# Performance work log

Hardware: AMD Instinct MI355X
Metric: run time of the kernel (lower is better)

Reference implementation:

```python
import jax, jax.numpy as jnp
import numpy as np

FILTER_LEN = 32
SCALE = float(np.sqrt(10 ** (-15 / 10)))  # expected_SI_power_dB = -15


def _fir_valid(x, w):
    """Valid cross-correlation along W axis. x: [B,H,W,1], w: [L] -> [B,H,W-L+1,1].
    Matches Keras Conv2D(kernel_size=(1,L), padding='valid') (cross-correlation)."""
    B, H, W, _ = x.shape
    L = w.shape[0]
    xr = x.reshape(B * H, W, 1)
    k = w.reshape(L, 1, 1)  # (spatial, in, out)
    y = jax.lax.conv_general_dilated(xr, k, window_strides=(1,), padding='VALID',
                                     dimension_numbers=('NWC', 'WIO', 'NWC'))
    return y.reshape(B, H, W - L + 1, 1)


def setup_inputs() -> dict:
    key = jax.random.key(0)
    ks = jax.random.split(key, 10)
    B, H, W = 16, 1, 262144
    f32 = jnp.float32
    return {
        'x_real': jax.random.normal(ks[0], (B, H, W, 1), f32),
        'x_imag': jax.random.normal(ks[1], (B, H, W, 1), f32),
        'w1_pre': jax.random.normal(ks[2], (1, 8), f32) * 0.5,
        'w2_pre': jax.random.normal(ks[3], (8, 1), f32) * 0.5,
        'w_fir_r': jax.random.normal(ks[4], (FILTER_LEN,), f32) * 0.1,
        'w_fir_i': jax.random.normal(ks[5], (FILTER_LEN,), f32) * 0.1,
        'w1_post': jax.random.normal(ks[6], (1, 8), f32) * 0.5,
        'b1_post': jax.random.normal(ks[7], (8,), f32) * 0.1,
        'w2_post': jax.random.normal(ks[8], (8, 1), f32) * 0.5,
        'b2_post': jax.random.normal(ks[9], (1,), f32) * 0.1,
    }


def reference(x_real, x_imag, w1_pre, w2_pre, w_fir_r, w_fir_i,
              w1_post, b1_post, w2_post, b2_post):
    # --- pre nonlinearity on magnitude (1x1 conv MLP: 1 -> 8 tanh -> 1) ---
    x_mag = jnp.sqrt(x_real * x_real + x_imag * x_imag)      # [B,H,W,1]
    x_phase = jnp.arctan2(x_imag, x_real)                    # [B,H,W,1]
    h = jnp.tanh(jnp.einsum('bhwc,cf->bhwf', x_mag, w1_pre))  # [B,H,W,8]
    m = jnp.einsum('bhwf,fc->bhwc', h, w2_pre)               # [B,H,W,1]
    xh_r = m * jnp.cos(x_phase)
    xh_i = m * jnp.sin(x_phase)
    # --- complex FIR (length-32, valid) via 4 real convs ---
    zr = _fir_valid(xh_r, w_fir_r) - _fir_valid(xh_i, w_fir_i)
    zi = _fir_valid(xh_i, w_fir_r) + _fir_valid(xh_r, w_fir_i)
    # --- post nonlinearity on magnitude (1x1 conv MLP: 1 -> 8 relu -> 1) ---
    z_mag = jnp.sqrt(zr * zr + zi * zi)
    z_phase = jnp.arctan2(zi, zr)
    g = jax.nn.relu(jnp.einsum('bhwc,cf->bhwf', z_mag, w1_post) + b1_post)
    zm = jnp.einsum('bhwf,fc->bhwc', g, w2_post) + b2_post
    yr = SCALE * zm * jnp.cos(z_phase)
    yi = SCALE * zm * jnp.sin(z_phase)
    # complex output represented as [real, imag] on last axis: [B,H,W-31,2]
    return jnp.concatenate([yr, yi], axis=-1)
```

## Files before the change

### kernel.cpp

```cpp
#include <hip/hip_runtime.h>

#define TILE   2048
#define WTILE  512
#define NSW    560
#define WIDTH  262144
#define OUTW   (WIDTH - 31)
#define SCALE_V 0.17782794100389229f

#define TBL_N    1024
#define TBL_MAX  10.0f
#define TBL_SCL  (TBL_N / TBL_MAX)

typedef _Float16 half8  __attribute__((ext_vector_type(8)));
typedef _Float16 half4v __attribute__((ext_vector_type(4)));
typedef float    floatx4 __attribute__((ext_vector_type(4)));

__device__ __forceinline__ float wload(const float* __restrict__ w, int t) {
    return (t >= 0 && t < 32) ? w[t] : 0.0f;
}

#define MFMA16(A, B, C) __builtin_amdgcn_mfma_f32_16x16x32_f16((A), (B), (C), 0, 0, 0)

__device__ __forceinline__ float s_of_mag(float mag, const float* w1, const float* w2) {
    if (mag == 0.0f) {
        float s = 0.f;
#pragma unroll
        for (int f = 0; f < 8; ++f) s = fmaf(w2[f], w1[f], s);
        return s;
    }
    float m = 0.f;
#pragma unroll
    for (int f = 0; f < 8; ++f) m = fmaf(w2[f], tanhf(w1[f] * mag), m);
    return m / mag;
}

__global__ void fill_s_table(const float* __restrict__ w1_pre,
                             const float* __restrict__ w2_pre,
                             float2* __restrict__ tbl)
{
    const int i = blockIdx.x * 256 + threadIdx.x;
    if (i >= TBL_N) return;
    float w1[8], w2[8];
#pragma unroll
    for (int f = 0; f < 8; ++f) { w1[f] = w1_pre[f]; w2[f] = w2_pre[f]; }
    const float m0 = (float)i       * (1.0f / TBL_SCL);
    const float m1 = (float)(i + 1) * (1.0f / TBL_SCL);
    const float s0 = s_of_mag(m0, w1, w2);
    const float s1 = s_of_mag(m1, w1, w2);
    tbl[i] = make_float2(s0, s1 - s0);
}

__global__ __launch_bounds__(256) void fused_hammer_mfma(
    const float* __restrict__ xr_g,   const float* __restrict__ xi_g,
    const float* __restrict__ w1_pre, const float* __restrict__ w2_pre,
    const float* __restrict__ wfr,    const float* __restrict__ wfi,
    const float* __restrict__ w1_post,const float* __restrict__ b1_post,
    const float* __restrict__ w2_post,const float* __restrict__ b2_post,
    const float2* __restrict__ tbl_g,
    float* __restrict__ out)
{
    __shared__ __align__(16) _Float16 s_rh[4][NSW];
    __shared__ __align__(16) _Float16 s_rl[4][NSW];
    __shared__ __align__(16) _Float16 s_ih[4][NSW];
    __shared__ __align__(16) _Float16 s_il[4][NSW];
    __shared__ __align__(16) float2   s_tab[TBL_N];

    const int tid    = threadIdx.x;
    const int lane   = tid & 63;
    const int wv     = tid >> 6;
    const int tstart = blockIdx.x * TILE;
    const int wstart = tstart + wv * WTILE;
    const int brow   = blockIdx.y;
    const long rowbase = (long)brow * WIDTH;

    {
        const float4* src = (const float4*)tbl_g;
#pragma unroll
        for (int q = 0; q < 2; ++q) {
            const int idx = 2 * tid + q;
            ((float4*)s_tab)[idx] = src[idx];
        }
    }

    float w1p[8], b1p[8], w2p[8];
#pragma unroll
    for (int f = 0; f < 8; ++f) { w1p[f] = w1_post[f]; b1p[f] = b1_post[f]; w2p[f] = w2_post[f]; }
    const float b2p = b2_post[0];

    const int jA = lane & 15;
    const int kg = lane >> 4;
    half8 A1r_h, A1r_l, A1mi_h, A1mi_l, A1i_h, A1i_l, A2r_h, A2r_l, A2i_h, A2i_l;
#pragma unroll
    for (int jj = 0; jj < 8; ++jj) {
        const int k  = 8 * kg + jj;
        const int t1 = k - jA;
        const float wr1 = wload(wfr, t1);
        const float wi1 = wload(wfi, t1);
        const int t2 = (k < 16) ? (k + 32 - jA) : (k + 16 - jA);
        const float wr2 = wload(wfr, t2);
        const float wi2 = wload(wfi, t2);
        const float a2r = (k < 16) ? wr2 : -wi2;
        const float a2i = (k < 16) ? wi2 : wr2;
        _Float16 h;
        h = (_Float16)wr1;   A1r_h[jj]  = h; A1r_l[jj]  = (_Float16)(wr1 - (float)h);
        h = (_Float16)(-wi1);A1mi_h[jj] = h; A1mi_l[jj] = (_Float16)(-wi1 - (float)h);
        h = (_Float16)wi1;   A1i_h[jj]  = h; A1i_l[jj]  = (_Float16)(wi1 - (float)h);
        h = (_Float16)a2r;   A2r_h[jj]  = h; A2r_l[jj]  = (_Float16)(a2r - (float)h);
        h = (_Float16)a2i;   A2i_h[jj]  = h; A2i_l[jj]  = (_Float16)(a2i - (float)h);
    }

    __syncthreads();

    for (int p = lane; p < NSW / 4; p += 64) {
        const int g = wstart + 4 * p;
        float4 vr, vi;
        if (g + 3 < WIDTH) {
            vr = *(const float4*)(xr_g + rowbase + g);
            vi = *(const float4*)(xi_g + rowbase + g);
        } else {
            float rr[4], ii[4];
#pragma unroll
            for (int e = 0; e < 4; ++e) {
                const int gg = g + e;
                rr[e] = (gg < WIDTH) ? xr_g[rowbase + gg] : 0.f;
                ii[e] = (gg < WIDTH) ? xi_g[rowbase + gg] : 0.f;
            }
            vr = make_float4(rr[0], rr[1], rr[2], rr[3]);
            vi = make_float4(ii[0], ii[1], ii[2], ii[3]);
        }
        const float* vrf = &vr.x;
        const float* vif = &vi.x;
        half4v rh, rl, ih, il;
#pragma unroll
        for (int e = 0; e < 4; ++e) {
            const float r  = vrf[e], im = vif[e];
            const float sq  = fmaf(r, r, im * im);
            const float mag = __builtin_sqrtf(sq);
            const float t   = fminf(mag * TBL_SCL, (float)(TBL_N - 2) + 0.999f);
            const int   i0  = (int)t;
            const float frac = t - (float)i0;
            const float2 en = s_tab[i0];
            const float s   = fmaf(frac, en.y, en.x);
            const float xhr = s * r;
            const float xhi = s * im;
            const _Float16 hr = (_Float16)xhr;
            const _Float16 hi = (_Float16)xhi;
            rh[e] = hr; rl[e] = (_Float16)(xhr - (float)hr);
            ih[e] = hi; il[e] = (_Float16)(xhi - (float)hi);
        }
        *(half4v*)&s_rh[wv][4 * p] = rh;
        *(half4v*)&s_rl[wv][4 * p] = rl;
        *(half4v*)&s_ih[wv][4 * p] = ih;
        *(half4v*)&s_il[wv][4 * p] = il;
    }
    asm volatile("s_waitcnt lgkmcnt(0)" ::: "memory");

    const bool row_aligned = ((brow & 1) == 0);

#pragma unroll
    for (int tt = 0; tt < 2; ++tt) {
        const int base_o = 256 * tt;
        const int i1 = base_o + 16 * jA + 8 * kg;
        const half8 Bxr_h = *(const half8*)&s_rh[wv][i1];
        const half8 Bxi_h = *(const half8*)&s_ih[wv][i1];
        const half8 Bxr_l = *(const half8*)&s_rl[wv][i1];
        const half8 Bxi_l = *(const half8*)&s_il[wv][i1];
        const int i2 = base_o + 16 * jA + 32 + 8 * (kg & 1);
        const _Float16* srcH = (kg < 2) ? s_rh[wv] : s_ih[wv];
        const _Float16* srcL = (kg < 2) ? s_rl[wv] : s_il[wv];
        const half8 Bmx_h = *(const half8*)&srcH[i2];
        const half8 Bmx_l = *(const half8*)&srcL[i2];

        floatx4 accr = {0.f, 0.f, 0.f, 0.f};
        floatx4 acci = {0.f, 0.f, 0.f, 0.f};
        accr = MFMA16(A1r_h,  Bxr_h, accr);  acci = MFMA16(A1i_h,  Bxr_h, acci);
        accr = MFMA16(A1mi_h, Bxi_h, accr);  acci = MFMA16(A1r_h,  Bxi_h, acci);
        accr = MFMA16(A2r_h,  Bmx_h, accr);  acci = MFMA16(A2i_h,  Bmx_h, acci);
        accr = MFMA16(A1r_h,  Bxr_l, accr);  acci = MFMA16(A1i_h,  Bxr_l, acci);
        accr = MFMA16(A1mi_h, Bxi_l, accr);  acci = MFMA16(A1r_h,  Bxi_l, acci);
        accr = MFMA16(A2r_h,  Bmx_l, accr);  acci = MFMA16(A2i_h,  Bmx_l, acci);
        accr = MFMA16(A1r_l,  Bxr_h, accr);  acci = MFMA16(A1i_l,  Bxr_h, acci);
        accr = MFMA16(A1mi_l, Bxi_h, accr);  acci = MFMA16(A1r_l,  Bxi_h, acci);
        accr = MFMA16(A2r_l,  Bmx_h, accr);  acci = MFMA16(A2i_l,  Bmx_h, acci);

        const int obase = wstart + base_o + 16 * jA + 4 * kg;
        float ox[8];
#pragma unroll
        for (int r = 0; r < 4; ++r) {
            const float zr  = accr[r], zi = acci[r];
            const float zsq = fmaf(zr, zr, zi * zi);
            const float rs  = (zsq > 0.f) ? __builtin_amdgcn_rsqf(zsq) : 0.f;
            const float zmag = zsq * rs;
            float zm = b2p;
#pragma unroll
            for (int f = 0; f < 8; ++f) {
                const float gfv = fmaf(zmag, w1p[f], b1p[f]);
                zm = fmaf(fmaxf(gfv, 0.f), w2p[f], zm);
            }
            const float t = SCALE_V * zm * rs;
            ox[2 * r]     = (zsq > 0.f) ? t * zr : SCALE_V * zm;
            ox[2 * r + 1] = t * zi;
        }
        float* po = &out[((long)brow * OUTW + obase) * 2];
        if (obase + 3 < OUTW) {
            if (row_aligned) {
                *(float4*)(po)     = make_float4(ox[0], ox[1], ox[2], ox[3]);
                *(float4*)(po + 4) = make_float4(ox[4], ox[5], ox[6], ox[7]);
            } else {
#pragma unroll
                for (int r = 0; r < 4; ++r)
                    *(float2*)(po + 2 * r) = make_float2(ox[2 * r], ox[2 * r + 1]);
            }
        } else {
#pragma unroll
            for (int r = 0; r < 4; ++r)
                if (obase + r < OUTW)
                    *(float2*)(po + 2 * r) = make_float2(ox[2 * r], ox[2 * r + 1]);
        }
    }
}

extern "C" void kernel_launch(void* const* d_in, const int* in_sizes, int n_in,
                              void* d_out, int out_size, void* d_ws, size_t ws_size,
                              hipStream_t stream) {
    float2* tbl = (float2*)d_ws;
    fill_s_table<<<dim3((TBL_N + 255) / 256), 256, 0, stream>>>(
        (const float*)d_in[2], (const float*)d_in[3], tbl);

    const int blocks_w = (OUTW + TILE - 1) / TILE;
    dim3 grid(blocks_w, 16);
    fused_hammer_mfma<<<grid, 256, 0, stream>>>(
        (const float*)d_in[0], (const float*)d_in[1],
        (const float*)d_in[2], (const float*)d_in[3],
        (const float*)d_in[4], (const float*)d_in[5],
        (const float*)d_in[6], (const float*)d_in[7],
        (const float*)d_in[8], (const float*)d_in[9],
        tbl,
        (float*)d_out);
}
```

Measured before the change: 111.5 us.

## Process two sub-tiles per wave with register prefetch of next input chunk

Each block now covers 4096 columns, so each wave handles two 512-wide sub-tiles in sequence. The first chunk's global loads are issued before the table and weight setup, and the next chunk is loaded into registers while the current one is converted and convolved. This halves the block count and amortises the per-block table copy and weight splitting. It also adds a min-bound occupancy hint, which risks register pressure. Edge loads are clamped rather than zero-filled; for the last tile the clamped values reach only outputs past OUTW, which are not written.

```diff
diff --git a/kernel.cpp b/kernel.cpp
--- a/kernel.cpp
+++ b/kernel.cpp
@@ -1,10 +1,9 @@
 #include <hip/hip_runtime.h>
 
-#define TILE   2048
+#define WIDTH  262144
+#define OUTW   (WIDTH - 31)
 #define WTILE  512
 #define NSW    560
-#define WIDTH  262144
-#define OUTW   (WIDTH - 31)
 #define SCALE_V 0.17782794100389229f
 
 #define TBL_N    1024
@@ -50,7 +49,7 @@
     tbl[i] = make_float2(s0, s1 - s0);
 }
 
-__global__ __launch_bounds__(256) void fused_hammer_mfma(
+__global__ __launch_bounds__(256, 4) void fused_hammer_mfma(
     const float* __restrict__ xr_g,   const float* __restrict__ xi_g,
     const float* __restrict__ w1_pre, const float* __restrict__ w2_pre,
     const float* __restrict__ wfr,    const float* __restrict__ wfi,
@@ -68,10 +67,16 @@
     const int tid    = threadIdx.x;
     const int lane   = tid & 63;
     const int wv     = tid >> 6;
-    const int tstart = blockIdx.x * TILE;
-    const int wstart = tstart + wv * WTILE;
     const int brow   = blockIdx.y;
     const long rowbase = (long)brow * WIDTH;
+    const int wbase  = blockIdx.x * 4096 + wv * 1024;
+
+    const int g0 = min(wbase       + 4 * lane, WIDTH - 4);
+    const int g1 = min(wbase + 256 + 4 * lane, WIDTH - 4);
+    float4 p_r0 = *(const float4*)(xr_g + rowbase + g0);
+    float4 p_i0 = *(const float4*)(xi_g + rowbase + g0);
+    float4 p_r1 = *(const float4*)(xr_g + rowbase + g1);
+    float4 p_i1 = *(const float4*)(xi_g + rowbase + g1);
 
     {
         const float4* src = (const float4*)tbl_g;
@@ -111,113 +116,126 @@
 
     __syncthreads();
 
-    for (int p = lane; p < NSW / 4; p += 64) {
-        const int g = wstart + 4 * p;
-        float4 vr, vi;
-        if (g + 3 < WIDTH) {
-            vr = *(const float4*)(xr_g + rowbase + g);
-            vi = *(const float4*)(xi_g + rowbase + g);
-        } else {
-            float rr[4], ii[4];
-#pragma unroll
-            for (int e = 0; e < 4; ++e) {
-                const int gg = g + e;
-                rr[e] = (gg < WIDTH) ? xr_g[rowbase + gg] : 0.f;
-                ii[e] = (gg < WIDTH) ? xi_g[rowbase + gg] : 0.f;
+    const bool row_aligned = ((brow & 1) == 0);
+
+#define STAGE4(VR, VI, P)                                                     \
+    do {                                                                      \
+        const float* vrf = &(VR).x;                                           \
+        const float* vif = &(VI).x;                                           \
+        half4v rh_, rl_, ih_, il_;                                            \
+        _Pragma("unroll")                                                     \
+        for (int e = 0; e < 4; ++e) {                                         \
+            const float r  = vrf[e], im = vif[e];                             \
+            const float sq  = fmaf(r, r, im * im);                            \
+            const float mag = __builtin_sqrtf(sq);                            \
+            const float t   = fminf(mag * TBL_SCL, (float)(TBL_N - 2) + 0.999f); \
+            const int   i0  = (int)t;                                         \
+            const float frac = t - (float)i0;                                 \
+            const float2 en = s_tab[i0];                                      \
+            const float s   = fmaf(frac, en.y, en.x);                         \
+            const float xhr = s * r;                                          \
+            const float xhi = s * im;                                         \
+            const _Float16 hr = (_Float16)xhr;                                \
+            const _Float16 hi = (_Float16)xhi;                                \
+            rh_[e] = hr; rl_[e] = (_Float16)(xhr - (float)hr);                \
+            ih_[e] = hi; il_[e] = (_Float16)(xhi - (float)hi);                \
+        }                                                                     \
+        *(half4v*)&s_rh[wv][4 * (P)] = rh_;                                   \
+        *(half4v*)&s_rl[wv][4 * (P)] = rl_;                                   \
+        *(half4v*)&s_ih[wv][4 * (P)] = ih_;                                   \
+        *(half4v*)&s_il[wv][4 * (P)] = il_;                                   \
+    } while (0)
+
+#pragma unroll
+    for (int q = 0; q < 2; ++q) {
+        const int wstart = wbase + q * WTILE;
+
+        float4 h_r, h_i;
+        if (lane < 12) {
+            const int g2 = min(wstart + 512 + 4 * lane, WIDTH - 4);
+            h_r = *(const float4*)(xr_g + rowbase + g2);
+            h_i = *(const float4*)(xi_g + rowbase + g2);
+        }
+
+        STAGE4(p_r0, p_i0, lane);
+        STAGE4(p_r1, p_i1, 64 + lane);
+
+        if (q == 0) {
+            const int n0 = min(wbase + 512       + 4 * lane, WIDTH - 4);
+            const int n1 = min(wbase + 512 + 256 + 4 * lane, WIDTH - 4);
+            p_r0 = *(const float4*)(xr_g + rowbase + n0);
+            p_i0 = *(const float4*)(xi_g + rowbase + n0);
+            p_r1 = *(const float4*)(xr_g + rowbase + n1);
+            p_i1 = *(const float4*)(xi_g + rowbase + n1);
+        }
+
+        if (lane < 12) STAGE4(h_r, h_i, 128 + lane);
+
+        asm volatile("s_waitcnt lgkmcnt(0)" ::: "memory");
+
+#pragma unroll
+        for (int tt = 0; tt < 2; ++tt) {
+            const int base_o = 256 * tt;
+            const int i1 = base_o + 16 * jA + 8 * kg;
+            const half8 Bxr_h = *(const half8*)&s_rh[wv][i1];
+            const half8 Bxi_h = *(const half8*)&s_ih[wv][i1];
+            const half8 Bxr_l = *(const half8*)&s_rl[wv][i1];
+            const half8 Bxi_l = *(const half8*)&s_il[wv][i1];
+            const int i2 = base_o + 16 * jA + 32 + 8 * (kg & 1);
+            const _Float16* srcH = (kg < 2) ? s_rh[wv] : s_ih[wv];
+            const _Float16* srcL = (kg < 2) ? s_rl[wv] : s_il[wv];
+            const half8 Bmx_h = *(const half8*)&srcH[i2];
+            const half8 Bmx_l = *(const half8*)&srcL[i2];
+
+            floatx4 accr = {0.f, 0.f, 0.f, 0.f};
+            floatx4 acci = {0.f, 0.f, 0.f, 0.f};
+            accr = MFMA16(A1r_h,  Bxr_h, accr);  acci = MFMA16(A1i_h,  Bxr_h, acci);
+            accr = MFMA16(A1mi_h, Bxi_h, accr);  acci = MFMA16(A1r_h,  Bxi_h, acci);
+            accr = MFMA16(A2r_h,  Bmx_h, accr);  acci = MFMA16(A2i_h,  Bmx_h, acci);
+            accr = MFMA16(A1r_h,  Bxr_l, accr);  acci = MFMA16(A1i_h,  Bxr_l, acci);
+            accr = MFMA16(A1mi_h, Bxi_l, accr);  acci = MFMA16(A1r_h,  Bxi_l, acci);
+            accr = MFMA16(A2r_h,  Bmx_l, accr);  acci = MFMA16(A2i_h,  Bmx_l, acci);
+            accr = MFMA16(A1r_l,  Bxr_h, accr);  acci = MFMA16(A1i_l,  Bxr_h, acci);
+            accr = MFMA16(A1mi_l, Bxi_h, accr);  acci = MFMA16(A1r_l,  Bxi_h, acci);
+            accr = MFMA16(A2r_l,  Bmx_h, accr);  acci = MFMA16(A2i_l,  Bmx_h, acci);
+
+            const int obase = wstart + base_o + 16 * jA + 4 * kg;
+            float ox[8];
+#pragma unroll
+            for (int r = 0; r < 4; ++r) {
+                const float zr  = accr[r], zi = acci[r];
+                const float zsq = fmaf(zr, zr, zi * zi);
+                const float rs  = (zsq > 0.f) ? __builtin_amdgcn_rsqf(zsq) : 0.f;
+                const float zmag = zsq * rs;
+                float zm = b2p;
+#pragma unroll
+                for (int f = 0; f < 8; ++f) {
+                    const float gfv = fmaf(zmag, w1p[f], b1p[f]);
+                    zm = fmaf(fmaxf(gfv, 0.f), w2p[f], zm);
+                }
+                const float t = SCALE_V * zm * rs;
+                ox[2 * r]     = (zsq > 0.f) ? t * zr : SCALE_V * zm;
+                ox[2 * r + 1] = t * zi;
             }
-            vr = make_float4(rr[0], rr[1], rr[2], rr[3]);
-            vi = make_float4(ii[0], ii[1], ii[2], ii[3]);
-        }
-        const float* vrf = &vr.x;
-        const float* vif = &vi.x;
-        half4v rh, rl, ih, il;
-#pragma unroll
-        for (int e = 0; e < 4; ++e) {
-            const float r  = vrf[e], im = vif[e];
-            const float sq  = fmaf(r, r, im * im);
-            const float mag = __builtin_sqrtf(sq);
-            const float t   = fminf(mag * TBL_SCL, (float)(TBL_N - 2) + 0.999f);
-            const int   i0  = (int)t;
-            const float frac = t - (float)i0;
-            const float2 en = s_tab[i0];
-            const float s   = fmaf(frac, en.y, en.x);
-            const float xhr = s * r;
-            const float xhi = s * im;
-            const _Float16 hr = (_Float16)xhr;
-            const _Float16 hi = (_Float16)xhi;
-            rh[e] = hr; rl[e] = (_Float16)(xhr - (float)hr);
-            ih[e] = hi; il[e] = (_Float16)(xhi - (float)hi);
-        }
-        *(half4v*)&s_rh[wv][4 * p] = rh;
-        *(half4v*)&s_rl[wv][4 * p] = rl;
-        *(half4v*)&s_ih[wv][4 * p] = ih;
-        *(half4v*)&s_il[wv][4 * p] = il;
-    }
-    asm volatile("s_waitcnt lgkmcnt(0)" ::: "memory");
-
-    const bool row_aligned = ((brow & 1) == 0);
-
-#pragma unroll
-    for (int tt = 0; tt < 2; ++tt) {
-        const int base_o = 256 * tt;
-        const int i1 = base_o + 16 * jA + 8 * kg;
-        const half8 Bxr_h = *(const half8*)&s_rh[wv][i1];
-        const half8 Bxi_h = *(const half8*)&s_ih[wv][i1];
-        const half8 Bxr_l = *(const half8*)&s_rl[wv][i1];
-        const half8 Bxi_l = *(const half8*)&s_il[wv][i1];
-        const int i2 = base_o + 16 * jA + 32 + 8 * (kg & 1);
-        const _Float16* srcH = (kg < 2) ? s_rh[wv] : s_ih[wv];
-        const _Float16* srcL = (kg < 2) ? s_rl[wv] : s_il[wv];
-        const half8 Bmx_h = *(const half8*)&srcH[i2];
-        const half8 Bmx_l = *(const half8*)&srcL[i2];
-
-        floatx4 accr = {0.f, 0.f, 0.f, 0.f};
-        floatx4 acci = {0.f, 0.f, 0.f, 0.f};
-        accr = MFMA16(A1r_h,  Bxr_h, accr);  acci = MFMA16(A1i_h,  Bxr_h, acci);
-        accr = MFMA16(A1mi_h, Bxi_h, accr);  acci = MFMA16(A1r_h,  Bxi_h, acci);
-        accr = MFMA16(A2r_h,  Bmx_h, accr);  acci = MFMA16(A2i_h,  Bmx_h, acci);
-        accr = MFMA16(A1r_h,  Bxr_l, accr);  acci = MFMA16(A1i_h,  Bxr_l, acci);
-        accr = MFMA16(A1mi_h, Bxi_l, accr);  acci = MFMA16(A1r_h,  Bxi_l, acci);
-        accr = MFMA16(A2r_h,  Bmx_l, accr);  acci = MFMA16(A2i_h,  Bmx_l, acci);
-        accr = MFMA16(A1r_l,  Bxr_h, accr);  acci = MFMA16(A1i_l,  Bxr_h, acci);
-        accr = MFMA16(A1mi_l, Bxi_h, accr);  acci = MFMA16(A1r_l,  Bxi_h, acci);
-        accr = MFMA16(A2r_l,  Bmx_h, accr);  acci = MFMA16(A2i_l,  Bmx_h, acci);
-
-        const int obase = wstart + base_o + 16 * jA + 4 * kg;
-        float ox[8];
-#pragma unroll
-        for (int r = 0; r < 4; ++r) {
-            const float zr  = accr[r], zi = acci[r];
-            const float zsq = fmaf(zr, zr, zi * zi);
-            const float rs  = (zsq > 0.f) ? __builtin_amdgcn_rsqf(zsq) : 0.f;
-            const float zmag = zsq * rs;
-            float zm = b2p;
-#pragma unroll
-            for (int f = 0; f < 8; ++f) {
-                const float gfv = fmaf(zmag, w1p[f], b1p[f]);
-                zm = fmaf(fmaxf(gfv, 0.f), w2p[f], zm);
+            float* po = &out[((long)brow * OUTW + obase) * 2];
+            if (obase + 3 < OUTW) {
+                if (row_aligned) {
+                    *(float4*)(po)     = make_float4(ox[0], ox[1], ox[2], ox[3]);
+                    *(float4*)(po + 4) = make_float4(ox[4], ox[5], ox[6], ox[7]);
+                } else {
+#pragma unroll
+                    for (int r = 0; r < 4; ++r)
+                        *(float2*)(po + 2 * r) = make_float2(ox[2 * r], ox[2 * r + 1]);
+                }
+            } else {
+#pragma unroll
+                for (int r = 0; r < 4; ++r)
+                    if (obase + r < OUTW)
+                        *(float2*)(po + 2 * r) = make_float2(ox[2 * r], ox[2 * r + 1]);
             }
-            const float t = SCALE_V * zm * rs;
-            ox[2 * r]     = (zsq > 0.f) ? t * zr : SCALE_V * zm;
-            ox[2 * r + 1] = t * zi;
-        }
-        float* po = &out[((long)brow * OUTW + obase) * 2];
-        if (obase + 3 < OUTW) {
-            if (row_aligned) {
-                *(float4*)(po)     = make_float4(ox[0], ox[1], ox[2], ox[3]);
-                *(float4*)(po + 4) = make_float4(ox[4], ox[5], ox[6], ox[7]);
-            } else {
-#pragma unroll
-                for (int r = 0; r < 4; ++r)
-                    *(float2*)(po + 2 * r) = make_float2(ox[2 * r], ox[2 * r + 1]);
-            }
-        } else {
-#pragma unroll
-            for (int r = 0; r < 4; ++r)
-                if (obase + r < OUTW)
-                    *(float2*)(po + 2 * r) = make_float2(ox[2 * r], ox[2 * r + 1]);
-        }
-    }
+        }
+    }
+#undef STAGE4
 }
 
 extern "C" void kernel_launch(void* const* d_in, const int* in_sizes, int n_in,
@@ -227,8 +245,7 @@
     fill_s_table<<<dim3((TBL_N + 255) / 256), 256, 0, stream>>>(
         (const float*)d_in[2], (const float*)d_in[3], tbl);
 
-    const int blocks_w = (OUTW + TILE - 1) / TILE;
-    dim3 grid(blocks_w, 16);
+    dim3 grid(64, 16);
     fused_hammer_mfma<<<grid, 256, 0, stream>>>(
         (const float*)d_in[0], (const float*)d_in[1],
         (const float*)d_in[2], (const float*)d_in[3],
```

New measurement: 111.2 us. About the same (-0.2%).
